# Kernel tuning notes

Measured on AMD Instinct MI355X. Metric: run time of the kernel, lower is better.

Reference implementation:

```python
import jax, jax.numpy as jnp
import numpy as np
from jax import lax

DIM = 2048
HEAD_DIM = 128
N_HEADS = 16
N_KV_HEADS = 4
N_REP = N_HEADS // N_KV_HEADS
K_CHUNK = 8          # token_chunk
SEQ = 2048
BATCH = 1
ROPE_THETA = 10000.0
KV_DIM = N_KV_HEADS * HEAD_DIM  # 512


def _make_freq_cis(seq, hd, theta):
    # (seq, hd//2, 2, 2) rotation matrices [[cos, -sin], [sin, cos]]
    inv = 1.0 / (theta ** (np.arange(0, hd, 2, dtype=np.float64) / hd))
    ang = np.outer(np.arange(seq, dtype=np.float64), inv)
    cos, sin = np.cos(ang), np.sin(ang)
    f = np.stack([np.stack([cos, -sin], -1), np.stack([sin, cos], -1)], -2)
    return jnp.asarray(f, jnp.float32)


def setup_inputs() -> dict:
    key = jax.random.key(0)
    ks = jax.random.split(key, 12)
    s = 0.02
    inp = {
        'x': jax.random.normal(ks[0], (BATCH, SEQ, DIM), jnp.float32),
        'freq_cis': _make_freq_cis(SEQ, HEAD_DIM, ROPE_THETA),
        # nn.Linear weights stored as (out, in); y = x @ W.T
        'wq': jax.random.normal(ks[1], (N_HEADS * HEAD_DIM, DIM), jnp.float32) * s,
        'wk': jax.random.normal(ks[2], (KV_DIM, DIM), jnp.float32) * s,
        'wv': jax.random.normal(ks[3], (KV_DIM, DIM), jnp.float32) * s,
        'wo': jax.random.normal(ks[4], (DIM, N_HEADS * HEAD_DIM), jnp.float32) * s,
        # diagonal SSM params for k_ssm / v_ssm (per-channel)
        'a_log_k': jax.random.normal(ks[5], (KV_DIM,), jnp.float32) * 0.5,
        'b_k': jax.random.normal(ks[6], (KV_DIM,), jnp.float32),
        'c_k': jax.random.normal(ks[7], (KV_DIM,), jnp.float32),
        'a_log_v': jax.random.normal(ks[8], (KV_DIM,), jnp.float32) * 0.5,
        'b_v': jax.random.normal(ks[9], (KV_DIM,), jnp.float32),
        'c_v': jax.random.normal(ks[10], (KV_DIM,), jnp.float32),
    }
    return inp


def _ssm_chunked(x, a_log, b, c):
    # Chunked diagonal SSM with state reset every K_CHUNK tokens
    # (equivalent to flat_process_chunks_with_ssm with boundaries every K).
    bsz, S, E = x.shape
    nc = S // K_CHUNK
    a = jnp.exp(-jax.nn.softplus(a_log))  # (E,) decay in (0, 1)
    xs = x.reshape(bsz * nc, K_CHUNK, E).swapaxes(0, 1)  # (K, N, E)

    def step(h, xt):
        h = a * h + b * xt
        return h, c * h

    _, ys = lax.scan(step, jnp.zeros((bsz * nc, E), x.dtype), xs)
    return ys.swapaxes(0, 1).reshape(bsz, S, E)


def _apply_rope(xq, xk, freq_cis):
    # xq: (b, s, h, hd); freq_cis: (s, hd//2, 2, 2)
    def rot(t):
        b, s, h, hd = t.shape
        tr = t.reshape(b, s, h, hd // 2, 1, 2)
        f = freq_cis.reshape(1, s, 1, hd // 2, 2, 2)
        return (tr * f).sum(-1).reshape(b, s, h, hd)
    return rot(xq), rot(xk)


def _forward(x, freq_cis, wq, wk, wv, wo, a_log_k, b_k, c_k, a_log_v, b_v, c_v):
    bsz, S, _ = x.shape
    xq = jnp.einsum('bsd,ed->bse', x, wq)
    xk = jnp.einsum('bsd,ed->bse', x, wk)
    xv = jnp.einsum('bsd,ed->bse', x, wv)

    # chunked SSM preprocessing of K/V (+ residual_ssm)
    xk_p = _ssm_chunked(xk, a_log_k, b_k, c_k) + xk
    xv_p = _ssm_chunked(xv, a_log_v, b_v, c_v) + xv

    xq = xq.reshape(bsz, S, N_HEADS, HEAD_DIM)
    xk_p = xk_p.reshape(bsz, S, N_KV_HEADS, HEAD_DIM)
    xv_p = xv_p.reshape(bsz, S, N_KV_HEADS, HEAD_DIM)

    xq, xk_p = _apply_rope(xq, xk_p, freq_cis)

    # GQA repeat_kv (torch.repeat_interleave on head dim)
    xk_p = jnp.repeat(xk_p, N_REP, axis=2)
    xv_p = jnp.repeat(xv_p, N_REP, axis=2)

    # chunk-boundary attention mask
    k_pos = jnp.arange(S)
    boundary = (k_pos % K_CHUNK) == (K_CHUNK - 1)
    t = jnp.arange(S)[:, None]
    k = k_pos[None, :]
    mask = ((k < t) & boundary[None, :]) | (k == t - 1) | ((k < 4) & (k <= t))

    q = xq.transpose(0, 2, 1, 3)   # (b, h, s, d)
    kk = xk_p.transpose(0, 2, 1, 3)
    vv = xv_p.transpose(0, 2, 1, 3)

    scores = jnp.einsum('bhqd,bhkd->bhqk', q, kk) / jnp.sqrt(
        jnp.asarray(HEAD_DIM, q.dtype))
    scores = jnp.where(mask[None, None], scores, -jnp.inf)
    attn = jax.nn.softmax(scores, axis=-1)
    out = jnp.einsum('bhqk,bhkd->bhqd', attn, vv)
    out = out.transpose(0, 2, 1, 3).reshape(bsz, S, N_HEADS * HEAD_DIM)
    return jnp.einsum('bse,de->bsd', out, wo)


def reference(x, freq_cis, wq, wk, wv, wo, a_log_k, b_k, c_k,
              a_log_v, b_v, c_v):
    return _forward(x, freq_cis, wq, wk, wv, wo,
                    a_log_k, b_k, c_k, a_log_v, b_v, c_v)
```

## Files before the change

kernel.cpp:

```cpp
#include <hip/hip_runtime.h>

typedef __bf16 bf16x8 __attribute__((ext_vector_type(8)));
typedef float  f32x4  __attribute__((ext_vector_type(4)));
typedef unsigned short u16;
typedef unsigned int   u32;

__device__ __forceinline__ float b2f(u16 u) {
    u32 x = ((u32)u) << 16;
    return __builtin_bit_cast(float, x);
}
__device__ __forceinline__ u16 f2b(float f) {
    u32 x = __builtin_bit_cast(u32, f);
    x += 0x7fffu + ((x >> 16) & 1u);
    return (u16)(x >> 16);
}

__global__ void convert_kernel(const float* __restrict__ x, const float* __restrict__ wq,
                               const float* __restrict__ wk, const float* __restrict__ wv,
                               const float* __restrict__ wo,
                               u16* __restrict__ xb, u16* __restrict__ wcat, u16* __restrict__ wob)
{
    long i4 = (long)blockIdx.x * 256 + threadIdx.x;
    long e = i4 * 4;
    const float* src; u16* dst;
    if (e < 4194304) { src = x + e; dst = xb + e; }
    else if (e < 10485760) {
        long j = e - 4194304;
        dst = wcat + j;
        if (j < 4194304)      src = wq + j;
        else if (j < 5242880) src = wk + (j - 4194304);
        else                  src = wv + (j - 5242880);
    } else {
        long j = e - 10485760;
        src = wo + j; dst = wob + j;
    }
    float4 v = *(const float4*)src;
    uint2 pk;
    pk.x = (u32)f2b(v.x) | ((u32)f2b(v.y) << 16);
    pk.y = (u32)f2b(v.z) | ((u32)f2b(v.w) << 16);
    *(uint2*)dst = pk;
}

template<int OUT_BF16>
__global__ __launch_bounds__(512) void gemm_bt_kernel(
    const u16* __restrict__ A, const u16* __restrict__ B,
    void* __restrict__ Cout, int M, int N, int K)
{
    __shared__ u16 As[2][8192];
    __shared__ u16 Bs[2][8192];
    const int tid  = threadIdx.x;
    const int lane = tid & 63;
    const int wave = tid >> 6;
    const int waveM = wave >> 2, waveN = wave & 3;
    const int tm = blockIdx.y * 128;
    const int tn = blockIdx.x * 128;

    f32x4 acc[4][2];
#pragma unroll
    for (int i = 0; i < 4; ++i)
#pragma unroll
        for (int j = 0; j < 2; ++j) acc[i][j] = f32x4{0.f, 0.f, 0.f, 0.f};

    const int frow = lane & 15;
    const int fk   = (lane >> 4) * 8;

    auto STAGE = [&](int buf, int kt) {
#pragma unroll
        for (int c = 0; c < 2; ++c) {
            int idx = c * 512 + tid;
            int row = idx >> 3;
            int blk = (idx & 7) ^ (row & 7);
            const u16* srcA = A + (size_t)(tm + row) * K + kt + blk * 8;
            const u16* srcB = B + (size_t)(tn + row) * K + kt + blk * 8;
            u16* dstA = &As[buf][(size_t)(c * 512 + wave * 64) * 8];
            u16* dstB = &Bs[buf][(size_t)(c * 512 + wave * 64) * 8];
            __builtin_amdgcn_global_load_lds((const __attribute__((address_space(1))) void*)srcA,
                                             (__attribute__((address_space(3))) void*)dstA, 16, 0, 0);
            __builtin_amdgcn_global_load_lds((const __attribute__((address_space(1))) void*)srcB,
                                             (__attribute__((address_space(3))) void*)dstB, 16, 0, 0);
        }
    };
    auto COMPUTE = [&](int buf) {
#pragma unroll
        for (int kk = 0; kk < 64; kk += 32) {
            bf16x8 af[4], bfr[2];
#pragma unroll
            for (int m = 0; m < 4; ++m) {
                int r  = waveM * 64 + m * 16 + frow;
                int kb_ = ((kk + fk) >> 3) ^ (r & 7);
                af[m] = *(const bf16x8*)&As[buf][r * 64 + kb_ * 8];
            }
#pragma unroll
            for (int n = 0; n < 2; ++n) {
                int r  = waveN * 32 + n * 16 + frow;
                int kb_ = ((kk + fk) >> 3) ^ (r & 7);
                bfr[n] = *(const bf16x8*)&Bs[buf][r * 64 + kb_ * 8];
            }
#pragma unroll
            for (int m = 0; m < 4; ++m)
#pragma unroll
                for (int n = 0; n < 2; ++n)
                    acc[m][n] = __builtin_amdgcn_mfma_f32_16x16x32_bf16(af[m], bfr[n], acc[m][n], 0, 0, 0);
        }
    };

    STAGE(0, 0);
    __syncthreads();
    int cur = 0;
    for (int kt = 64; kt < K; kt += 64) {
        STAGE(cur ^ 1, kt);
        COMPUTE(cur);
        __syncthreads();
        cur ^= 1;
    }
    COMPUTE(cur);

    const int rb = tm + waveM * 64;
    const int cb = tn + waveN * 32;
#pragma unroll
    for (int m = 0; m < 4; ++m)
#pragma unroll
        for (int n = 0; n < 2; ++n)
#pragma unroll
            for (int r = 0; r < 4; ++r) {
                int row = rb + m * 16 + (lane >> 4) * 4 + r;
                int col = cb + n * 16 + (lane & 15);
                if (OUT_BF16) ((u16*)Cout)[(size_t)row * N + col] = f2b(acc[m][n][r]);
                else          ((float*)Cout)[(size_t)row * N + col] = acc[m][n][r];
            }
}

__global__ void ssm_rope_kernel(const u16* __restrict__ c1, const float* __restrict__ fc,
                                const float* __restrict__ alk, const float* __restrict__ bk,
                                const float* __restrict__ ck,
                                const float* __restrict__ alv, const float* __restrict__ bv,
                                const float* __restrict__ cv,
                                u16* __restrict__ qb, u16* __restrict__ kb, u16* __restrict__ vb)
{
    int gi = blockIdx.x * 256 + threadIdx.x;
    if (gi < 2097152) {
        int s = gi >> 10, pg = gi & 1023;
        int i = pg & 63;
        int e0 = (pg >> 6) * 128 + 2 * i;
        u32 u = *(const u32*)&c1[(size_t)s * 3072 + e0];
        float x0 = b2f((u16)(u & 0xffff)), x1 = b2f((u16)(u >> 16));
        float4 f = *(const float4*)&fc[((size_t)s * 64 + i) * 4];
        float q0 = x0 * f.x - x1 * f.z;
        float q1 = x0 * f.z + x1 * f.x;
        *(u32*)&qb[(size_t)s * 2048 + e0] = (u32)f2b(q0) | ((u32)f2b(q1) << 16);
    } else if (gi < 2097152 + 65536) {
        int ki = gi - 2097152;
        int chunk = ki >> 8, pr = ki & 255;
        int i = pr & 63;
        int e0 = (pr >> 6) * 128 + 2 * i;
        float z0 = alk[e0], z1 = alk[e0 + 1];
        float sp0 = z0 > 20.f ? z0 : log1pf(__expf(z0));
        float sp1 = z1 > 20.f ? z1 : log1pf(__expf(z1));
        float a0 = __expf(-sp0), a1 = __expf(-sp1);
        float b0 = bk[e0], b1 = bk[e0 + 1];
        float c0 = ck[e0], cc1 = ck[e0 + 1];
        float h0 = 0.f, h1 = 0.f;
#pragma unroll
        for (int tt = 0; tt < 8; ++tt) {
            int s = chunk * 8 + tt;
            u32 u = *(const u32*)&c1[(size_t)s * 3072 + 2048 + e0];
            float x0 = b2f((u16)(u & 0xffff)), x1 = b2f((u16)(u >> 16));
            h0 = a0 * h0 + b0 * x0;
            h1 = a1 * h1 + b1 * x1;
            float y0 = c0 * h0 + x0;
            float y1 = cc1 * h1 + x1;
            float4 f = *(const float4*)&fc[((size_t)s * 64 + i) * 4];
            float k0 = y0 * f.x - y1 * f.z;
            float k1 = y0 * f.z + y1 * f.x;
            *(u32*)&kb[(size_t)s * 512 + e0] = (u32)f2b(k0) | ((u32)f2b(k1) << 16);
        }
    } else {
        int vi = gi - 2097152 - 65536;
        int chunk = vi >> 9, e = vi & 511;
        float z = alv[e];
        float sp = z > 20.f ? z : log1pf(__expf(z));
        float a = __expf(-sp);
        float b = bv[e], c = cv[e];
        float h = 0.f;
#pragma unroll
        for (int tt = 0; tt < 8; ++tt) {
            int s = chunk * 8 + tt;
            float xvv = b2f(c1[(size_t)s * 3072 + 2560 + e]);
            h = a * h + b * xvv;
            vb[(size_t)s * 512 + e] = f2b(c * h + xvv);
        }
    }
}

__global__ void compact_kernel(const u16* __restrict__ kb, const u16* __restrict__ vb,
                               u16* __restrict__ kbc, u16* __restrict__ vbt)
{
    int id = blockIdx.x * 256 + threadIdx.x;
    int kvh = id >> 15, rem = id & 32767, j = rem >> 7, d = rem & 127;
    int src = (8 * j + 7) * 512 + kvh * 128 + d;
    kbc[(((kvh << 8) + j) << 7) + d] = kb[src];
    vbt[(((kvh << 7) + d) << 8) + j] = vb[src];
}

__global__ __launch_bounds__(512, 2) void attn_kernel(
    const u16* __restrict__ qb, const u16* __restrict__ kb, const u16* __restrict__ vb,
    const u16* __restrict__ kbc, const u16* __restrict__ vbt, u16* __restrict__ aout)
{
    __shared__ u16   ksbuf[32768];
    __shared__ u16   vsbuf[32768];
    __shared__ float p_ext[8][16][32];

    const int tid  = threadIdx.x;
    const int w    = tid >> 6;
    const int lane = tid & 63;
    const int s    = lane & 15;
    const int g    = lane >> 4;
    const int h    = blockIdx.x >> 4;
    const int t0   = (blockIdx.x & 15) * 128;
    const int kvh  = h >> 2;
    const int qw   = t0 + w * 16;

    {
        const u16* kcb = kbc + ((size_t)kvh << 15);
#pragma unroll
        for (int it = 0; it < 8; ++it) {
            int idx = it * 512 + tid;
            int r = idx >> 4, b = idx & 15;
            const u16* src = kcb + r * 128 + ((b ^ (r & 7)) << 3);
            u16* dst = ksbuf + (size_t)(it * 512 + w * 64) * 8;
            __builtin_amdgcn_global_load_lds((const __attribute__((address_space(1))) void*)src,
                                             (__attribute__((address_space(3))) void*)dst, 16, 0, 0);
        }
    }
    __syncthreads();

    {
        const u16* vtb = vbt + ((size_t)kvh << 15);
#pragma unroll
        for (int it = 0; it < 8; ++it) {
            int idx = it * 512 + tid;
            int r = idx >> 5, b = idx & 31;
            const u16* src = vtb + r * 256 + ((b ^ (r & 7)) << 3);
            u16* dst = vsbuf + (size_t)(it * 512 + w * 64) * 8;
            __builtin_amdgcn_global_load_lds((const __attribute__((address_space(1))) void*)src,
                                             (__attribute__((address_space(3))) void*)dst, 16, 0, 0);
        }
    }

    bf16x8 qa[4];
    {
        const u16* qr = qb + (size_t)(qw + s) * 2048 + h * 128 + g * 8;
#pragma unroll
        for (int kk = 0; kk < 4; ++kk) qa[kk] = *(const bf16x8*)&qr[kk * 32];
    }

    f32x4 sf[18];
#pragma unroll
    for (int i = 0; i < 18; ++i) sf[i] = f32x4{0.f, 0.f, 0.f, 0.f};

#pragma unroll
    for (int fb = 0; fb < 16; ++fb) {
        int row = fb * 16 + s;
#pragma unroll
        for (int kk = 0; kk < 4; ++kk) {
            int ch = (kk * 4 + g) ^ (s & 7);
            bf16x8 bf = *(const bf16x8*)&ksbuf[row * 128 + ch * 8];
            sf[fb] = __builtin_amdgcn_mfma_f32_16x16x32_bf16(qa[kk], bf, sf[fb], 0, 0, 0);
        }
    }
#pragma unroll
    for (int xb = 0; xb < 2; ++xb) {
        int i = xb * 16 + s;
        int keyrow = (i < 4) ? i : (qw + (i - 4) - 1);
        if (keyrow < 0) keyrow = 0;
        if (keyrow > 2047) keyrow = 2047;
        const u16* kr = kb + (size_t)keyrow * 512 + kvh * 128 + g * 8;
#pragma unroll
        for (int kk = 0; kk < 4; ++kk) {
            bf16x8 bf = *(const bf16x8*)&kr[kk * 32];
            sf[16 + xb] = __builtin_amdgcn_mfma_f32_16x16x32_bf16(qa[kk], bf, sf[16 + xb], 0, 0, 0);
        }
    }

    const float scale = 0.08838834764831845f;
    float mx[4] = {-1e30f, -1e30f, -1e30f, -1e30f};
#pragma unroll
    for (int fi = 0; fi < 18; ++fi)
#pragma unroll
        for (int r = 0; r < 4; ++r) {
            int q = g * 4 + r;
            int t = qw + q;
            bool ok;
            if (fi < 16) {
                int j = fi * 16 + s;
                ok = j < (t >> 3);
            } else {
                int i = (fi - 16) * 16 + s;
                if (i < 4) ok = (i <= t);
                else       ok = ((i - 4) == q) && ((t & 7) != 0) && (t >= 5);
            }
            float v = ok ? sf[fi][r] * scale : -1e30f;
            sf[fi][r] = v;
            mx[r] = fmaxf(mx[r], v);
        }
#pragma unroll
    for (int r = 0; r < 4; ++r)
#pragma unroll
        for (int off = 8; off; off >>= 1) mx[r] = fmaxf(mx[r], __shfl_xor(mx[r], off));

    float sm[4] = {0.f, 0.f, 0.f, 0.f};
#pragma unroll
    for (int fi = 0; fi < 18; ++fi)
#pragma unroll
        for (int r = 0; r < 4; ++r) {
            float p = __expf(sf[fi][r] - mx[r]);
            sf[fi][r] = p;
            sm[r] += p;
        }
#pragma unroll
    for (int r = 0; r < 4; ++r)
#pragma unroll
        for (int off = 8; off; off >>= 1) sm[r] += __shfl_xor(sm[r], off);
    float inv[4];
#pragma unroll
    for (int r = 0; r < 4; ++r) inv[r] = 1.f / sm[r];

    __syncthreads();

    u16* pbuf = ksbuf + w * 4096;
#pragma unroll
    for (int fi = 0; fi < 16; ++fi)
#pragma unroll
        for (int r = 0; r < 4; ++r) {
            int q = g * 4 + r;
            int c = fi * 16 + s;
            int blk = (c >> 3) ^ q;
            pbuf[q * 256 + (blk << 3) + (c & 7)] = f2b(sf[fi][r]);
        }
#pragma unroll
    for (int xb = 0; xb < 2; ++xb)
#pragma unroll
        for (int r = 0; r < 4; ++r)
            p_ext[w][g * 4 + r][xb * 16 + s] = sf[16 + xb][r];

    bf16x8 pa[8];
#pragma unroll
    for (int kk = 0; kk < 8; ++kk) {
        int blk = (kk * 4 + g) ^ s;
        pa[kk] = *(const bf16x8*)&pbuf[s * 256 + (blk << 3)];
    }
    f32x4 out[8];
#pragma unroll
    for (int f = 0; f < 8; ++f) out[f] = f32x4{0.f, 0.f, 0.f, 0.f};
#pragma unroll
    for (int f = 0; f < 8; ++f) {
        int row = f * 16 + s;
#pragma unroll
        for (int kk = 0; kk < 8; ++kk) {
            int ch = (kk * 4 + g) ^ (s & 7);
            bf16x8 vf = *(const bf16x8*)&vsbuf[row * 256 + ch * 8];
            out[f] = __builtin_amdgcn_mfma_f32_16x16x32_bf16(pa[kk], vf, out[f], 0, 0, 0);
        }
    }

    {
        float v4[4][8];
#pragma unroll
        for (int e = 0; e < 4; ++e)
#pragma unroll
            for (int f = 0; f < 8; ++f)
                v4[e][f] = b2f(vb[(size_t)e * 512 + kvh * 128 + f * 16 + s]);
#pragma unroll
        for (int r = 0; r < 4; ++r) {
            int q = g * 4 + r;
            int t = qw + q;
#pragma unroll
            for (int e = 0; e < 4; ++e) {
                float p = p_ext[w][q][e];
#pragma unroll
                for (int f = 0; f < 8; ++f) out[f][r] += p * v4[e][f];
            }
            float pp = p_ext[w][q][4 + q];
            int key = t - 1; if (key < 0) key = 0;
            const u16* vr = vb + (size_t)key * 512 + kvh * 128;
#pragma unroll
            for (int f = 0; f < 8; ++f) out[f][r] += pp * b2f(vr[f * 16 + s]);
        }
    }

#pragma unroll
    for (int f = 0; f < 8; ++f)
#pragma unroll
        for (int r = 0; r < 4; ++r) {
            int t = qw + g * 4 + r;
            aout[(size_t)t * 2048 + h * 128 + f * 16 + s] = f2b(out[f][r] * inv[r]);
        }
}

extern "C" void kernel_launch(void* const* d_in, const int* in_sizes, int n_in,
                              void* d_out, int out_size, void* d_ws, size_t ws_size,
                              hipStream_t stream) {
    const float* x   = (const float*)d_in[0];
    const float* fc  = (const float*)d_in[1];
    const float* wq  = (const float*)d_in[2];
    const float* wk  = (const float*)d_in[3];
    const float* wv  = (const float*)d_in[4];
    const float* wo  = (const float*)d_in[5];
    const float* alk = (const float*)d_in[6];
    const float* bk  = (const float*)d_in[7];
    const float* ck  = (const float*)d_in[8];
    const float* alv = (const float*)d_in[9];
    const float* bv  = (const float*)d_in[10];
    const float* cv  = (const float*)d_in[11];

    char* ws = (char*)d_ws;
    u16*   xb   = (u16*)(ws);
    u16*   wcat = (u16*)(ws + 8388608);
    u16*   wob  = (u16*)(ws + 20971520);
    u16*   c1   = (u16*)(ws + 29360128);
    u16*   qb   = (u16*)(ws + 54525952);
    u16*   kb   = (u16*)(ws + 62914560);
    u16*   vb   = (u16*)(ws + 65011712);
    u16*   kbc  = (u16*)(ws + 67108864);
    u16*   vbt  = (u16*)(ws + 67371008);
    u16*   aout = (u16*)(ws + 67633152);

    convert_kernel<<<14336, 256, 0, stream>>>(x, wq, wk, wv, wo, xb, wcat, wob);

    dim3 g1(3072 / 128, 2048 / 128);
    gemm_bt_kernel<1><<<g1, 512, 0, stream>>>(xb, wcat, (void*)c1, 2048, 3072, 2048);

    ssm_rope_kernel<<<8960, 256, 0, stream>>>(c1, fc, alk, bk, ck, alv, bv, cv, qb, kb, vb);

    compact_kernel<<<512, 256, 0, stream>>>(kb, vb, kbc, vbt);

    attn_kernel<<<256, 512, 0, stream>>>(qb, kb, vb, kbc, vbt, aout);

    dim3 g3(2048 / 128, 2048 / 128);
    gemm_bt_kernel<0><<<g3, 512, 0, stream>>>(aout, wob, d_out, 2048, 2048, 2048);
}
```

Measured before the change: 116.3 us.

## Triple-buffer GEMM LDS with vmcnt waits and XCD-aware tile remapping

Moves the GEMM main loop from two LDS buffers to three. It waits with explicit s_waitcnt vmcnt counts and raw s_barrier, so global loads for stage t+2 stay in flight while stage t computes and there is one barrier per iteration instead of a full sync. It also switches to a 1D grid and remaps block IDs so consecutive tiles on the same XCD (blockIdx mod 8) share rows and columns, which should improve L2 reuse. This raises LDS use to 96KB per block and relies on the staging loads issuing exactly 4 vmem ops, the hardcoded gridY=16 (M=2048), and the number of blocks being divisible by 8.

```diff
diff --git a/kernel.cpp b/kernel.cpp
--- a/kernel.cpp
+++ b/kernel.cpp
@@ -46,14 +46,21 @@
     const u16* __restrict__ A, const u16* __restrict__ B,
     void* __restrict__ Cout, int M, int N, int K)
 {
-    __shared__ u16 As[2][8192];
-    __shared__ u16 Bs[2][8192];
+    __shared__ u16 As[3][8192];
+    __shared__ u16 Bs[3][8192];
     const int tid  = threadIdx.x;
     const int lane = tid & 63;
     const int wave = tid >> 6;
     const int waveM = wave >> 2, waveN = wave & 3;
-    const int tm = blockIdx.y * 128;
-    const int tn = blockIdx.x * 128;
+
+    const int gridY = 16;
+    const int nwg   = (N >> 7) * gridY;
+    const int cpx   = nwg >> 3;
+    const int tile  = (blockIdx.x & 7) * cpx + (blockIdx.x >> 3);
+    const int by    = tile & (gridY - 1);
+    const int bx    = tile >> 4;
+    const int tm = by * 128;
+    const int tn = bx * 128;
 
     f32x4 acc[4][2];
 #pragma unroll
@@ -104,16 +111,24 @@
         }
     };
 
+    const int nk = K >> 6;
     STAGE(0, 0);
-    __syncthreads();
-    int cur = 0;
-    for (int kt = 64; kt < K; kt += 64) {
-        STAGE(cur ^ 1, kt);
-        COMPUTE(cur);
-        __syncthreads();
-        cur ^= 1;
-    }
-    COMPUTE(cur);
+    STAGE(1, 64);
+    for (int t = 0; t < nk - 2; ++t) {
+        asm volatile("s_waitcnt vmcnt(4)" ::: "memory");
+        __builtin_amdgcn_s_barrier();
+        __builtin_amdgcn_sched_barrier(0);
+        STAGE((t + 2) % 3, (t + 2) << 6);
+        COMPUTE(t % 3);
+    }
+    asm volatile("s_waitcnt vmcnt(4)" ::: "memory");
+    __builtin_amdgcn_s_barrier();
+    __builtin_amdgcn_sched_barrier(0);
+    COMPUTE((nk - 2) % 3);
+    asm volatile("s_waitcnt vmcnt(0)" ::: "memory");
+    __builtin_amdgcn_s_barrier();
+    __builtin_amdgcn_sched_barrier(0);
+    COMPUTE((nk - 1) % 3);
 
     const int rb = tm + waveM * 64;
     const int cb = tn + waveN * 32;
@@ -427,8 +442,7 @@
 
     convert_kernel<<<14336, 256, 0, stream>>>(x, wq, wk, wv, wo, xb, wcat, wob);
 
-    dim3 g1(3072 / 128, 2048 / 128);
-    gemm_bt_kernel<1><<<g1, 512, 0, stream>>>(xb, wcat, (void*)c1, 2048, 3072, 2048);
+    gemm_bt_kernel<1><<<384, 512, 0, stream>>>(xb, wcat, (void*)c1, 2048, 3072, 2048);
 
     ssm_rope_kernel<<<8960, 256, 0, stream>>>(c1, fc, alk, bk, ck, alv, bv, cv, qb, kb, vb);
 
@@ -436,6 +450,5 @@
 
     attn_kernel<<<256, 512, 0, stream>>>(qb, kb, vb, kbc, vbt, aout);
 
-    dim3 g3(2048 / 128, 2048 / 128);
-    gemm_bt_kernel<0><<<g3, 512, 0, stream>>>(aout, wob, d_out, 2048, 2048, 2048);
-}
+    gemm_bt_kernel<0><<<256, 512, 0, stream>>>(aout, wob, d_out, 2048, 2048, 2048);
+}
```

After: 174.3 us. 1.5x slower.
